# Optimization experiments

Hardware: AMD Instinct MI355X
Metric: run time of the kernel (lower is better)

## Reference

```python
import jax, jax.numpy as jnp
import numpy as np
import math

H = 8  # num_heads
# mock_theta_f Taylor coefficients: K(q) = 1 + q - 2q^2 + 3q^3
COEFFS = (1.0, 1.0, -2.0, 3.0)


def setup_inputs() -> dict:
    key = jax.random.key(0)
    ks = jax.random.split(key, 12)
    B, L, E = 2, 2048, 512
    s = 0.02
    return {
        "query": jax.random.normal(ks[0], (B, L, E), jnp.float32),
        "key_": jax.random.normal(ks[1], (B, L, E), jnp.float32),
        "value": jax.random.normal(ks[2], (B, L, E), jnp.float32),
        "Wq": jax.random.normal(ks[3], (E, E), jnp.float32) * s,
        "bq": jnp.zeros((E,), jnp.float32),
        "Wk": jax.random.normal(ks[4], (E, E), jnp.float32) * s,
        "bk": jnp.zeros((E,), jnp.float32),
        "Wv": jax.random.normal(ks[5], (E, E), jnp.float32) * s,
        "bv": jnp.zeros((E,), jnp.float32),
        "Wo": jax.random.normal(ks[6], (E, E), jnp.float32) * s,
        "bo": jnp.zeros((E,), jnp.float32),
        "log_tau": jnp.zeros((), jnp.float32),  # tau = exp(0) = 1.0
    }


def _horner(q):
    a0, a1, a2, a3 = COEFFS
    val = jnp.full_like(q, a3)
    val = q * val + a2
    val = q * val + a1
    val = q * val + a0
    return jnp.maximum(val, 0.0)


def _attn(query, key_, value, Wq, bq, Wk, bk, Wv, bv, Wo, bo, log_tau):
    B, L, E = query.shape
    S = key_.shape[1]
    Hd = E // H
    scale = math.sqrt(Hd)

    Q = (query @ Wq.T + bq).reshape(B, L, H, Hd).transpose(0, 2, 1, 3)  # (B,H,L,Hd)
    K = (key_ @ Wk.T + bk).reshape(B, S, H, Hd).transpose(0, 2, 1, 3)
    V = (value @ Wv.T + bv).reshape(B, S, H, Hd).transpose(0, 2, 1, 3)

    scores = jnp.einsum("bhld,bhsd->bhls", Q, K) / scale  # (B,H,L,S)

    tau = jnp.exp(log_tau)
    q = jax.nn.sigmoid(scores / tau)
    kv = _horner(q)

    # causal mask (is_causal=True): mask strict upper triangle
    causal = jnp.triu(jnp.ones((L, S), dtype=bool), k=1)  # (L,S)
    kv = jnp.where(causal[None, None], 0.0, kv)

    denom = jnp.sum(kv, axis=-1, keepdims=True)
    weights = kv / jnp.maximum(denom, 1e-12)

    out = jnp.einsum("bhls,bhsd->bhld", weights, V)  # (B,H,L,Hd)
    out = out.transpose(0, 2, 1, 3).reshape(B, L, E)
    return out @ Wo.T + bo


def reference(query, key_, value, Wq, bq, Wk, bk, Wv, bv, Wo, bo, log_tau):
    return _attn(query, key_, value, Wq, bq, Wk, bk, Wv, bv, Wo, bo, log_tau)
```

## Files before the change

### kernel.cpp

```cpp
#include <hip/hip_runtime.h>
#include <hip/hip_bf16.h>


typedef __attribute__((ext_vector_type(8))) __bf16 bf16x8;
typedef __attribute__((ext_vector_type(4))) __bf16 bf16x4;
typedef __attribute__((ext_vector_type(4))) float f32x4;
typedef __attribute__((ext_vector_type(4))) int i32x4;

#define NB 2
#define NL 2048
#define NE 512
#define NH 8
#define HD 64
#define NROW (NB * NL)
#define NJOB 144

__device__ __forceinline__ void gload16(const void* g, void* l) {
  __builtin_amdgcn_global_load_lds(
      (const __attribute__((address_space(1))) void*)g,
      (__attribute__((address_space(3))) void*)l, 16, 0, 0);
}

__global__ __launch_bounds__(256) void cvt_qkv(
    const float* __restrict__ q, const float* __restrict__ k,
    const float* __restrict__ v, __bf16* __restrict__ qo,
    __bf16* __restrict__ ko, __bf16* __restrict__ vo) {
  const int gid = blockIdx.x * 256 + threadIdx.x;
  const int seg = gid >> 19;
  const int i = gid & ((1 << 19) - 1);
  const float* s = seg == 0 ? q : (seg == 1 ? k : v);
  __bf16* d = seg == 0 ? qo : (seg == 1 ? ko : vo);
  float4 x = ((const float4*)s)[i];
  bf16x4 o = {(__bf16)x.x, (__bf16)x.y, (__bf16)x.z, (__bf16)x.w};
  ((bf16x4*)d)[i] = o;
}

__global__ __launch_bounds__(256) void cvt_w(
    const float* __restrict__ w0, const float* __restrict__ w1,
    const float* __restrict__ w2, const float* __restrict__ w3,
    __bf16* __restrict__ o0, __bf16* __restrict__ o1,
    __bf16* __restrict__ o2, __bf16* __restrict__ o3) {
  const int gid = blockIdx.x * 256 + threadIdx.x;
  const int seg = gid >> 16;
  const int i = gid & 0xFFFF;
  const float* s = seg == 0 ? w0 : (seg == 1 ? w1 : (seg == 2 ? w2 : w3));
  __bf16* d = seg == 0 ? o0 : (seg == 1 ? o1 : (seg == 2 ? o2 : o3));
  float4 x = ((const float4*)s)[i];
  bf16x4 o = {(__bf16)x.x, (__bf16)x.y, (__bf16)x.z, (__bf16)x.w};
  ((bf16x4*)d)[i] = o;
}

template <int MODE>
__device__ __forceinline__ void gemm_body(const __bf16* __restrict__ A,
                                          const __bf16* __restrict__ W,
                                          const float* __restrict__ bias,
                                          __bf16* __restrict__ outb,
                                          float* __restrict__ outf) {
  __shared__ __align__(16) __bf16 As[128 * 32];
  __shared__ __align__(16) __bf16 Ws[128 * 32];

  const int tid = threadIdx.x;
  const int lane = tid & 63, w = tid >> 6;
  const int lr = lane & 15, lg = lane >> 4;
  const int brow = blockIdx.y * 128, bcol = blockIdx.x * 128;
  const int wr = (w >> 1) * 64, wc = (w & 1) * 64;

  f32x4 zero4 = {0.f, 0.f, 0.f, 0.f};
  f32x4 acc[4][4];
#pragma unroll
  for (int i = 0; i < 4; ++i)
#pragma unroll
    for (int j = 0; j < 4; ++j) acc[i][j] = zero4;

  const int c0 = tid, c1 = tid + 256;
  const int r0 = c0 >> 2, cc0 = c0 & 3;
  const int r1 = c1 >> 2, cc1 = c1 & 3;

  for (int k0 = 0; k0 < NE; k0 += 32) {
    __syncthreads();
    gload16(A + (size_t)(brow + r0) * NE + k0 + cc0 * 8, As + c0 * 8);
    gload16(W + (size_t)(bcol + r0) * NE + k0 + cc0 * 8, Ws + c0 * 8);
    gload16(A + (size_t)(brow + r1) * NE + k0 + cc1 * 8, As + c1 * 8);
    gload16(W + (size_t)(bcol + r1) * NE + k0 + cc1 * 8, Ws + c1 * 8);
    __syncthreads();

    bf16x8 af[4], wf[4];
#pragma unroll
    for (int mi = 0; mi < 4; ++mi)
      af[mi] = *(const bf16x8*)(As + (wr + mi * 16 + lr) * 32 + lg * 8);
#pragma unroll
    for (int ni = 0; ni < 4; ++ni)
      wf[ni] = *(const bf16x8*)(Ws + (wc + ni * 16 + lr) * 32 + lg * 8);
#pragma unroll
    for (int mi = 0; mi < 4; ++mi)
#pragma unroll
      for (int ni = 0; ni < 4; ++ni)
        acc[mi][ni] = __builtin_amdgcn_mfma_f32_16x16x32_bf16(
            af[mi], wf[ni], acc[mi][ni], 0, 0, 0);
  }

#pragma unroll
  for (int mi = 0; mi < 4; ++mi) {
#pragma unroll
    for (int ni = 0; ni < 4; ++ni) {
      const int col = bcol + wc + ni * 16 + lr;
      const float bv = bias[col];
#pragma unroll
      for (int r = 0; r < 4; ++r) {
        const int row = brow + wr + mi * 16 + lg * 4 + r;
        const float v = acc[mi][ni][r] + bv;
        if (MODE == 0) {
          const int b = row >> 11, l = row & (NL - 1);
          const int h = col >> 6, d = col & 63;
          outb[(((size_t)b * NH + h) * NL + l) * HD + d] = (__bf16)v;
        } else if (MODE == 2) {
          const int b = row >> 11, l = row & (NL - 1);
          const int h = col >> 6, d = col & 63;
          outb[(((size_t)b * NH + h) * HD + d) * NL + l] = (__bf16)v;
        } else {
          outf[(size_t)row * NE + col] = v;
        }
      }
    }
  }
}

__global__ __launch_bounds__(256) void qkv_gemm(
    const __bf16* __restrict__ A0, const __bf16* __restrict__ A1,
    const __bf16* __restrict__ A2, const __bf16* __restrict__ W0,
    const __bf16* __restrict__ W1, const __bf16* __restrict__ W2,
    const float* __restrict__ b0, const float* __restrict__ b1,
    const float* __restrict__ b2, __bf16* __restrict__ O0,
    __bf16* __restrict__ O1, __bf16* __restrict__ O2) {
  const int z = blockIdx.z;
  if (z == 2) {
    gemm_body<2>(A2, W2, b2, O2, nullptr);
  } else {
    const __bf16* A = z == 0 ? A0 : A1;
    const __bf16* W = z == 0 ? W0 : W1;
    const float* bias = z == 0 ? b0 : b1;
    __bf16* O = z == 0 ? O0 : O1;
    gemm_body<0>(A, W, bias, O, nullptr);
  }
}

__global__ __launch_bounds__(256) void out_gemm(const __bf16* __restrict__ A,
                                                const __bf16* __restrict__ W,
                                                const float* __restrict__ bias,
                                                float* __restrict__ outf) {
  gemm_body<1>(A, W, bias, nullptr, outf);
}

template <int SLOTTED>
__global__ __launch_bounds__(256) void attn_kernel(
    const __bf16* __restrict__ Qg, const __bf16* __restrict__ Kg,
    const __bf16* __restrict__ VTg, float* __restrict__ numg,
    float* __restrict__ deng, const float* __restrict__ log_tau) {
  __shared__ __align__(16) __bf16 Kt[64][72];
  __shared__ __align__(16) __bf16 Vt[64][72];

  const int j = blockIdx.x;
  int qb, c;
  if (j < 32) {
    c = 0; qb = j;
  } else if (j < 60) {
    c = 1; qb = j - 28;
  } else if (j < 84) {
    c = 2; qb = j - 52;
  } else if (j < 104) {
    c = 3; qb = j - 72;
  } else if (j < 120) {
    c = 4; qb = j - 88;
  } else if (j < 132) {
    c = 5; qb = j - 100;
  } else if (j < 140) {
    c = 6; qb = j - 108;
  } else {
    c = 7; qb = j - 112;
  }
  const int bh = blockIdx.y;
  const __bf16* Qh = Qg + (size_t)bh * NL * HD;
  const __bf16* Kh = Kg + (size_t)bh * NL * HD;
  const __bf16* Vth = VTg + (size_t)bh * HD * NL;

  const int tid = threadIdx.x;
  const int lane = tid & 63, w = tid >> 6;
  const int lr = lane & 15, lg = lane >> 4;
  const float ninv = -1.44269504f / (8.0f * __expf(log_tau[0]));

  const int q0 = qb * 64;
  const int qg = q0 + w * 16 + lr;
  bf16x8 qf[2];
  qf[0] = *(const bf16x8*)(Qh + (size_t)qg * HD + lg * 8);
  qf[1] = *(const bf16x8*)(Qh + (size_t)qg * HD + 32 + lg * 8);

  f32x4 zero4 = {0.f, 0.f, 0.f, 0.f};
  f32x4 o_acc[4];
#pragma unroll
  for (int n = 0; n < 4; ++n) o_acc[n] = zero4;
  float den_l = 0.f;

  const int t0 = c * 4;
  const int t1 = min(t0 + 4, qb + 1);

  const int kr0 = tid >> 3, kc0 = (tid & 7) * 8;

  bf16x8 kpa = *(const bf16x8*)(Kh + (size_t)(t0 * 64 + kr0) * HD + kc0);
  bf16x8 kpb = *(const bf16x8*)(Kh + (size_t)(t0 * 64 + kr0 + 32) * HD + kc0);
  bf16x8 vpa = *(const bf16x8*)(Vth + (size_t)kr0 * NL + t0 * 64 + kc0);
  bf16x8 vpb = *(const bf16x8*)(Vth + (size_t)(kr0 + 32) * NL + t0 * 64 + kc0);

  const int idxA = (((lane & 16) << 1) + lr) * 4;
  const bool hi = (lane & 32) != 0;

  for (int t = t0; t < t1; ++t) {
    const int kv0 = t * 64;
    __syncthreads();
    *(bf16x8*)&Kt[kr0][kc0] = kpa;
    *(bf16x8*)&Kt[kr0 + 32][kc0] = kpb;
    *(bf16x8*)&Vt[kr0][kc0] = vpa;
    *(bf16x8*)&Vt[kr0 + 32][kc0] = vpb;
    __syncthreads();

    if (t + 1 < t1) {
      const int kn = (t + 1) * 64;
      kpa = *(const bf16x8*)(Kh + (size_t)(kn + kr0) * HD + kc0);
      kpb = *(const bf16x8*)(Kh + (size_t)(kn + kr0 + 32) * HD + kc0);
      vpa = *(const bf16x8*)(Vth + (size_t)kr0 * NL + kn + kc0);
      vpb = *(const bf16x8*)(Vth + (size_t)(kr0 + 32) * NL + kn + kc0);
    }

    f32x4 sacc[4];
#pragma unroll
    for (int si = 0; si < 4; ++si) sacc[si] = zero4;
#pragma unroll
    for (int kk = 0; kk < 2; ++kk) {
#pragma unroll
      for (int si = 0; si < 4; ++si) {
        bf16x8 kf = *(const bf16x8*)&Kt[si * 16 + lr][kk * 32 + lg * 8];
        sacc[si] = __builtin_amdgcn_mfma_f32_16x16x32_bf16(kf, qf[kk],
                                                           sacc[si], 0, 0, 0);
      }
    }

    unsigned pk[4][2];
#pragma unroll
    for (int si = 0; si < 4; ++si) {
      const int sb = kv0 + si * 16 + lg * 4;
      unsigned kbv[4];
#pragma unroll
      for (int r = 0; r < 4; ++r) {
        const float e = __builtin_amdgcn_exp2f(sacc[si][r] * ninv);
        const float qs = __builtin_amdgcn_rcpf(1.0f + e);
        float kvv = fmaf(qs, fmaf(qs, fmaf(qs, 3.0f, -2.0f), 1.0f), 1.0f);
        if (sb + r > qg) kvv = 0.0f;
        const __bf16 kb = (__bf16)kvv;
        den_l += (float)kb;
        kbv[r] = (unsigned)__builtin_bit_cast(unsigned short, kb);
      }
      pk[si][0] = kbv[0] | (kbv[1] << 16);
      pk[si][1] = kbv[2] | (kbv[3] << 16);
    }

#pragma unroll
    for (int kk = 0; kk < 2; ++kk) {
      const int sl = kk * 2, sh = kk * 2 + 1;
      const int a0 = __builtin_amdgcn_ds_bpermute(idxA, (int)pk[sl][0]);
      const int a1 = __builtin_amdgcn_ds_bpermute(idxA, (int)pk[sl][1]);
      const int b0 = __builtin_amdgcn_ds_bpermute(idxA + 64, (int)pk[sl][0]);
      const int b1 = __builtin_amdgcn_ds_bpermute(idxA + 64, (int)pk[sl][1]);
      const int c0 = __builtin_amdgcn_ds_bpermute(idxA, (int)pk[sh][0]);
      const int c1 = __builtin_amdgcn_ds_bpermute(idxA, (int)pk[sh][1]);
      const int d0 = __builtin_amdgcn_ds_bpermute(idxA + 64, (int)pk[sh][0]);
      const int d1 = __builtin_amdgcn_ds_bpermute(idxA + 64, (int)pk[sh][1]);
      i32x4 pw = {hi ? c0 : a0, hi ? c1 : a1, hi ? d0 : b0, hi ? d1 : b1};
      bf16x8 pf = __builtin_bit_cast(bf16x8, pw);
#pragma unroll
      for (int n = 0; n < 4; ++n) {
        bf16x8 vf = *(const bf16x8*)&Vt[n * 16 + lr][kk * 32 + lg * 8];
        o_acc[n] = __builtin_amdgcn_mfma_f32_16x16x32_bf16(pf, vf, o_acc[n],
                                                           0, 0, 0);
      }
    }
  }

  den_l += __shfl_xor(den_l, 16, 64);
  den_l += __shfl_xor(den_l, 32, 64);

  if (SLOTTED) {
    float* nslot = numg + (((size_t)bh * NJOB + j) << 12);
    const int lrow = w * 16 + lg * 4;
    if (lg == 0) {
      float* dslot = deng + (((size_t)bh * NJOB + j) << 6);
      dslot[w * 16 + lr] = den_l;
    }
#pragma unroll
    for (int n = 0; n < 4; ++n) {
      const int col = n * 16 + lr;
#pragma unroll
      for (int r = 0; r < 4; ++r) nslot[(lrow + r) * 64 + col] = o_acc[n][r];
    }
  } else {
    const int orow = q0 + w * 16 + lg * 4;
    if (lg == 0) atomicAdd(&deng[(size_t)bh * NL + q0 + w * 16 + lr], den_l);
#pragma unroll
    for (int n = 0; n < 4; ++n) {
      const int col = n * 16 + lr;
#pragma unroll
      for (int r = 0; r < 4; ++r)
        atomicAdd(&numg[((size_t)bh * NL + orow + r) * HD + col], o_acc[n][r]);
    }
  }
}

__global__ __launch_bounds__(256) void combine_slotted(
    const float* __restrict__ numS, const float* __restrict__ denS,
    __bf16* __restrict__ AO) {
  const int gid = blockIdx.x * 256 + threadIdx.x;
  const int d4 = gid & 15;
  const int row = gid >> 4;
  const int bh = row >> 11, l = row & (NL - 1);
  const int b = bh >> 3, h = bh & 7;
  const int qb = l >> 6, lrow = l & 63;
  const int nc = (qb >> 2) + 1;

  f32x4 acc = {0.f, 0.f, 0.f, 0.f};
  float d = 0.f;
  for (int c = 0; c < nc; ++c) {
    const int jj = qb + 2 * c * (15 - c);
    const size_t sb = (size_t)bh * NJOB + jj;
    acc += *(const f32x4*)(numS + ((sb << 6) + lrow) * 64 + d4 * 4);
    d += denS[(sb << 6) + lrow];
  }
  const float idv = __builtin_amdgcn_rcpf(fmaxf(d, 1e-12f));
  bf16x4 o = {(__bf16)(acc[0] * idv), (__bf16)(acc[1] * idv),
              (__bf16)(acc[2] * idv), (__bf16)(acc[3] * idv)};
  *(bf16x4*)&AO[((size_t)b * NL + l) * NE + h * HD + d4 * 4] = o;
}

__global__ __launch_bounds__(256) void combine_kernel(
    const float* __restrict__ numg, const float* __restrict__ deng,
    __bf16* __restrict__ AO) {
  const int gid = blockIdx.x * 256 + threadIdx.x;
  const int d4 = gid & 15;
  const int row = gid >> 4;
  const int bh = row >> 11, l = row & (NL - 1);
  const int b = bh >> 3, h = bh & 7;
  f32x4 n4 = ((const f32x4*)numg)[gid];
  const float idv = __builtin_amdgcn_rcpf(fmaxf(deng[row], 1e-12f));
  bf16x4 o = {(__bf16)(n4[0] * idv), (__bf16)(n4[1] * idv),
              (__bf16)(n4[2] * idv), (__bf16)(n4[3] * idv)};
  *(bf16x4*)&AO[((size_t)b * NL + l) * NE + h * HD + d4 * 4] = o;
}

extern "C" void kernel_launch(void* const* d_in, const int* in_sizes, int n_in,
                              void* d_out, int out_size, void* d_ws,
                              size_t ws_size, hipStream_t stream) {
  const float* query = (const float*)d_in[0];
  const float* key_ = (const float*)d_in[1];
  const float* value = (const float*)d_in[2];
  const float* Wq = (const float*)d_in[3];
  const float* bq = (const float*)d_in[4];
  const float* Wk = (const float*)d_in[5];
  const float* bk = (const float*)d_in[6];
  const float* Wv = (const float*)d_in[7];
  const float* bv = (const float*)d_in[8];
  const float* Wo = (const float*)d_in[9];
  const float* bo = (const float*)d_in[10];
  const float* log_tau = (const float*)d_in[11];

  char* ws = (char*)d_ws;
  const size_t MB = 1024 * 1024;
  const bool slotted = (ws_size >= 55 * MB);

  __bf16* xb = (__bf16*)(ws + 0 * MB);
  __bf16* kxb = (__bf16*)(ws + 4 * MB);
  __bf16* vxb = (__bf16*)(ws + 8 * MB);

  __bf16 *wqb, *wkb, *wvb, *wob, *Qh, *Kh, *VT, *AO;
  float *numb, *denb;
  if (slotted) {
    numb = (float*)(ws + 0 * MB);
    denb = (float*)(ws + 36 * MB);
    wqb = (__bf16*)(ws + 37 * MB);
    wkb = (__bf16*)(ws + 37 * MB + 512 * 1024);
    wvb = (__bf16*)(ws + 38 * MB);
    wob = (__bf16*)(ws + 38 * MB + 512 * 1024);
    Qh = (__bf16*)(ws + 39 * MB);
    Kh = (__bf16*)(ws + 43 * MB);
    VT = (__bf16*)(ws + 47 * MB);
    AO = (__bf16*)(ws + 51 * MB);
  } else {
    numb = (float*)(ws + 0 * MB);
    denb = (float*)(ws + 8 * MB);
    wqb = (__bf16*)(ws + 12 * MB);
    wkb = (__bf16*)(ws + 12 * MB + 512 * 1024);
    wvb = (__bf16*)(ws + 13 * MB);
    wob = (__bf16*)(ws + 13 * MB + 512 * 1024);
    Qh = (__bf16*)(ws + 14 * MB);
    Kh = (__bf16*)(ws + 18 * MB);
    VT = (__bf16*)(ws + 22 * MB);
    AO = (__bf16*)(ws + 26 * MB);
  }

  cvt_qkv<<<3 * (1 << 19) / 256, 256, 0, stream>>>(query, key_, value, xb, kxb,
                                                   vxb);
  cvt_w<<<4 * (1 << 16) / 256, 256, 0, stream>>>(Wq, Wk, Wv, Wo, wqb, wkb, wvb,
                                                 wob);

  dim3 gq(NE / 128, NROW / 128, 3);
  qkv_gemm<<<gq, 256, 0, stream>>>(xb, kxb, vxb, wqb, wkb, wvb, bq, bk, bv, Qh,
                                   Kh, VT);

  dim3 ga(NJOB, NB * NH);
  if (slotted) {
    attn_kernel<1><<<ga, 256, 0, stream>>>(Qh, Kh, VT, numb, denb, log_tau);
    combine_slotted<<<2048, 256, 0, stream>>>(numb, denb, AO);
  } else {
    hipMemsetAsync(ws, 0, 8 * MB + 128 * 1024, stream);
    attn_kernel<0><<<ga, 256, 0, stream>>>(Qh, Kh, VT, numb, denb, log_tau);
    combine_kernel<<<2048, 256, 0, stream>>>(numb, denb, AO);
  }

  dim3 gg(NE / 128, NROW / 128);
  out_gemm<<<gg, 256, 0, stream>>>(AO, wob, bo, (float*)d_out);
}
```

Measured before the change: 79.57 us.

## Process two query blocks per attention workgroup to reuse staged K/V tiles

New measurement: 83.53 us. 5.0% more time.

```diff
diff --git a/kernel.cpp b/kernel.cpp
--- a/kernel.cpp
+++ b/kernel.cpp
@@ -159,25 +159,18 @@
   __shared__ __align__(16) __bf16 Kt[64][72];
   __shared__ __align__(16) __bf16 Vt[64][72];
 
-  const int j = blockIdx.x;
-  int qb, c;
-  if (j < 32) {
-    c = 0; qb = j;
-  } else if (j < 60) {
-    c = 1; qb = j - 28;
-  } else if (j < 84) {
-    c = 2; qb = j - 52;
-  } else if (j < 104) {
-    c = 3; qb = j - 72;
-  } else if (j < 120) {
-    c = 4; qb = j - 88;
-  } else if (j < 132) {
-    c = 5; qb = j - 100;
-  } else if (j < 140) {
-    c = 6; qb = j - 108;
-  } else {
-    c = 7; qb = j - 112;
-  }
+  int jj = 71 - blockIdx.x;
+  int qi = 0, c = 0;
+  for (int k = 0; k < 16; ++k) {
+    const int n = (k >> 1) + 1;
+    if (jj < n) { qi = k; c = jj; break; }
+    jj -= n;
+  }
+  const int m2 = qi >> 1;
+  const int job = ((qi & 1) ? (m2 + 1) * (m2 + 1) : m2 * (m2 + 1)) + c;
+  const int qA = 2 * qi;
+  const int q0B = (qA + 1) * 64;
+
   const int bh = blockIdx.y;
   const __bf16* Qh = Qg + (size_t)bh * NL * HD;
   const __bf16* Kh = Kg + (size_t)bh * NL * HD;
@@ -188,20 +181,24 @@
   const int lr = lane & 15, lg = lane >> 4;
   const float ninv = -1.44269504f / (8.0f * __expf(log_tau[0]));
 
-  const int q0 = qb * 64;
-  const int qg = q0 + w * 16 + lr;
-  bf16x8 qf[2];
-  qf[0] = *(const bf16x8*)(Qh + (size_t)qg * HD + lg * 8);
-  qf[1] = *(const bf16x8*)(Qh + (size_t)qg * HD + 32 + lg * 8);
+  bf16x8 qf[2][2];
+#pragma unroll
+  for (int pp = 0; pp < 2; ++pp) {
+    const int qrow = q0B - pp * 64 + w * 16 + lr;
+    qf[pp][0] = *(const bf16x8*)(Qh + (size_t)qrow * HD + lg * 8);
+    qf[pp][1] = *(const bf16x8*)(Qh + (size_t)qrow * HD + 32 + lg * 8);
+  }
 
   f32x4 zero4 = {0.f, 0.f, 0.f, 0.f};
-  f32x4 o_acc[4];
-#pragma unroll
-  for (int n = 0; n < 4; ++n) o_acc[n] = zero4;
-  float den_l = 0.f;
+  f32x4 o_acc[2][4];
+#pragma unroll
+  for (int pp = 0; pp < 2; ++pp)
+#pragma unroll
+    for (int n = 0; n < 4; ++n) o_acc[pp][n] = zero4;
+  float den_l[2] = {0.f, 0.f};
 
   const int t0 = c * 4;
-  const int t1 = min(t0 + 4, qb + 1);
+  const int t1 = min(t0 + 4, 2 * qi + 2);
 
   const int kr0 = tid >> 3, kc0 = (tid & 7) * 8;
 
@@ -230,85 +227,105 @@
       vpb = *(const bf16x8*)(Vth + (size_t)(kr0 + 32) * NL + kn + kc0);
     }
 
-    f32x4 sacc[4];
-#pragma unroll
-    for (int si = 0; si < 4; ++si) sacc[si] = zero4;
-#pragma unroll
-    for (int kk = 0; kk < 2; ++kk) {
+#pragma unroll
+    for (int pp = 0; pp < 2; ++pp) {
+      if (pp == 1 && t > qA) continue;
+      const int qq = q0B - pp * 64 + w * 16 + lr;
+
+      f32x4 sacc[4];
+#pragma unroll
+      for (int si = 0; si < 4; ++si) sacc[si] = zero4;
+#pragma unroll
+      for (int kk = 0; kk < 2; ++kk) {
+#pragma unroll
+        for (int si = 0; si < 4; ++si) {
+          bf16x8 kf = *(const bf16x8*)&Kt[si * 16 + lr][kk * 32 + lg * 8];
+          sacc[si] = __builtin_amdgcn_mfma_f32_16x16x32_bf16(
+              kf, qf[pp][kk], sacc[si], 0, 0, 0);
+        }
+      }
+
+      unsigned pk[4][2];
 #pragma unroll
       for (int si = 0; si < 4; ++si) {
-        bf16x8 kf = *(const bf16x8*)&Kt[si * 16 + lr][kk * 32 + lg * 8];
-        sacc[si] = __builtin_amdgcn_mfma_f32_16x16x32_bf16(kf, qf[kk],
-                                                           sacc[si], 0, 0, 0);
+        const int sb = kv0 + si * 16 + lg * 4;
+        unsigned kbv[4];
+#pragma unroll
+        for (int r = 0; r < 4; ++r) {
+          const float e = __builtin_amdgcn_exp2f(sacc[si][r] * ninv);
+          const float qs = __builtin_amdgcn_rcpf(1.0f + e);
+          float kvv = fmaf(qs, fmaf(qs, fmaf(qs, 3.0f, -2.0f), 1.0f), 1.0f);
+          if (sb + r > qq) kvv = 0.0f;
+          const __bf16 kb = (__bf16)kvv;
+          den_l[pp] += (float)kb;
+          kbv[r] = (unsigned)__builtin_bit_cast(unsigned short, kb);
+        }
+        pk[si][0] = kbv[0] | (kbv[1] << 16);
+        pk[si][1] = kbv[2] | (kbv[3] << 16);
+      }
+
+#pragma unroll
+      for (int kk = 0; kk < 2; ++kk) {
+        const int sl = kk * 2, sh = kk * 2 + 1;
+        const int a0 = __builtin_amdgcn_ds_bpermute(idxA, (int)pk[sl][0]);
+        const int a1 = __builtin_amdgcn_ds_bpermute(idxA, (int)pk[sl][1]);
+        const int b0 = __builtin_amdgcn_ds_bpermute(idxA + 64, (int)pk[sl][0]);
+        const int b1 = __builtin_amdgcn_ds_bpermute(idxA + 64, (int)pk[sl][1]);
+        const int c0 = __builtin_amdgcn_ds_bpermute(idxA, (int)pk[sh][0]);
+        const int c1 = __builtin_amdgcn_ds_bpermute(idxA, (int)pk[sh][1]);
+        const int d0 = __builtin_amdgcn_ds_bpermute(idxA + 64, (int)pk[sh][0]);
+        const int d1 = __builtin_amdgcn_ds_bpermute(idxA + 64, (int)pk[sh][1]);
+        i32x4 pw = {hi ? c0 : a0, hi ? c1 : a1, hi ? d0 : b0, hi ? d1 : b1};
+        bf16x8 pf = __builtin_bit_cast(bf16x8, pw);
+#pragma unroll
+        for (int n = 0; n < 4; ++n) {
+          bf16x8 vf = *(const bf16x8*)&Vt[n * 16 + lr][kk * 32 + lg * 8];
+          o_acc[pp][n] = __builtin_amdgcn_mfma_f32_16x16x32_bf16(
+              pf, vf, o_acc[pp][n], 0, 0, 0);
+        }
       }
     }
-
-    unsigned pk[4][2];
-#pragma unroll
-    for (int si = 0; si < 4; ++si) {
-      const int sb = kv0 + si * 16 + lg * 4;
-      unsigned kbv[4];
-#pragma unroll
-      for (int r = 0; r < 4; ++r) {
-        const float e = __builtin_amdgcn_exp2f(sacc[si][r] * ninv);
-        const float qs = __builtin_amdgcn_rcpf(1.0f + e);
-        float kvv = fmaf(qs, fmaf(qs, fmaf(qs, 3.0f, -2.0f), 1.0f), 1.0f);
-        if (sb + r > qg) kvv = 0.0f;
-        const __bf16 kb = (__bf16)kvv;
-        den_l += (float)kb;
-        kbv[r] = (unsigned)__builtin_bit_cast(unsigned short, kb);
-      }
-      pk[si][0] = kbv[0] | (kbv[1] << 16);
-      pk[si][1] = kbv[2] | (kbv[3] << 16);
-    }
-
-#pragma unroll
-    for (int kk = 0; kk < 2; ++kk) {
-      const int sl = kk * 2, sh = kk * 2 + 1;
-      const int a0 = __builtin_amdgcn_ds_bpermute(idxA, (int)pk[sl][0]);
-      const int a1 = __builtin_amdgcn_ds_bpermute(idxA, (int)pk[sl][1]);
-      const int b0 = __builtin_amdgcn_ds_bpermute(idxA + 64, (int)pk[sl][0]);
-      const int b1 = __builtin_amdgcn_ds_bpermute(idxA + 64, (int)pk[sl][1]);
-      const int c0 = __builtin_amdgcn_ds_bpermute(idxA, (int)pk[sh][0]);
-      const int c1 = __builtin_amdgcn_ds_bpermute(idxA, (int)pk[sh][1]);
-      const int d0 = __builtin_amdgcn_ds_bpermute(idxA + 64, (int)pk[sh][0]);
-      const int d1 = __builtin_amdgcn_ds_bpermute(idxA + 64, (int)pk[sh][1]);
-      i32x4 pw = {hi ? c0 : a0, hi ? c1 : a1, hi ? d0 : b0, hi ? d1 : b1};
-      bf16x8 pf = __builtin_bit_cast(bf16x8, pw);
+  }
+
+#pragma unroll
+  for (int pp = 0; pp < 2; ++pp) {
+    den_l[pp] += __shfl_xor(den_l[pp], 16, 64);
+    den_l[pp] += __shfl_xor(den_l[pp], 32, 64);
+  }
+
+  if (SLOTTED) {
+#pragma unroll
+    for (int pp = 0; pp < 2; ++pp) {
+      const int slot = 2 * job + 1 - pp;
+      float* nslot = numg + (((size_t)bh * NJOB + slot) << 12);
+      const int lrow = w * 16 + lg * 4;
+      if (lg == 0) {
+        float* dslot = deng + (((size_t)bh * NJOB + slot) << 6);
+        dslot[w * 16 + lr] = den_l[pp];
+      }
 #pragma unroll
       for (int n = 0; n < 4; ++n) {
-        bf16x8 vf = *(const bf16x8*)&Vt[n * 16 + lr][kk * 32 + lg * 8];
-        o_acc[n] = __builtin_amdgcn_mfma_f32_16x16x32_bf16(pf, vf, o_acc[n],
-                                                           0, 0, 0);
-      }
-    }
-  }
-
-  den_l += __shfl_xor(den_l, 16, 64);
-  den_l += __shfl_xor(den_l, 32, 64);
-
-  if (SLOTTED) {
-    float* nslot = numg + (((size_t)bh * NJOB + j) << 12);
-    const int lrow = w * 16 + lg * 4;
-    if (lg == 0) {
-      float* dslot = deng + (((size_t)bh * NJOB + j) << 6);
-      dslot[w * 16 + lr] = den_l;
-    }
-#pragma unroll
-    for (int n = 0; n < 4; ++n) {
-      const int col = n * 16 + lr;
-#pragma unroll
-      for (int r = 0; r < 4; ++r) nslot[(lrow + r) * 64 + col] = o_acc[n][r];
+        const int col = n * 16 + lr;
+#pragma unroll
+        for (int r = 0; r < 4; ++r)
+          nslot[(lrow + r) * 64 + col] = o_acc[pp][n][r];
+      }
     }
   } else {
-    const int orow = q0 + w * 16 + lg * 4;
-    if (lg == 0) atomicAdd(&deng[(size_t)bh * NL + q0 + w * 16 + lr], den_l);
-#pragma unroll
-    for (int n = 0; n < 4; ++n) {
-      const int col = n * 16 + lr;
-#pragma unroll
-      for (int r = 0; r < 4; ++r)
-        atomicAdd(&numg[((size_t)bh * NL + orow + r) * HD + col], o_acc[n][r]);
+#pragma unroll
+    for (int pp = 0; pp < 2; ++pp) {
+      const int orow = q0B - pp * 64 + w * 16 + lg * 4;
+      if (lg == 0)
+        atomicAdd(&deng[(size_t)bh * NL + q0B - pp * 64 + w * 16 + lr],
+                  den_l[pp]);
+#pragma unroll
+      for (int n = 0; n < 4; ++n) {
+        const int col = n * 16 + lr;
+#pragma unroll
+        for (int r = 0; r < 4; ++r)
+          atomicAdd(&numg[((size_t)bh * NL + orow + r) * HD + col],
+                    o_acc[pp][n][r]);
+      }
     }
   }
 }
@@ -322,13 +339,15 @@
   const int bh = row >> 11, l = row & (NL - 1);
   const int b = bh >> 3, h = bh & 7;
   const int qb = l >> 6, lrow = l & 63;
+  const int qi = qb >> 1, par = qb & 1, m2 = qi >> 1;
+  const int jbase = (qi & 1) ? (m2 + 1) * (m2 + 1) : m2 * (m2 + 1);
   const int nc = (qb >> 2) + 1;
 
   f32x4 acc = {0.f, 0.f, 0.f, 0.f};
   float d = 0.f;
   for (int c = 0; c < nc; ++c) {
-    const int jj = qb + 2 * c * (15 - c);
-    const size_t sb = (size_t)bh * NJOB + jj;
+    const int slot = 2 * (jbase + c) + par;
+    const size_t sb = (size_t)bh * NJOB + slot;
     acc += *(const f32x4*)(numS + ((sb << 6) + lrow) * 64 + d4 * 4);
     d += denS[(sb << 6) + lrow];
   }
@@ -412,7 +431,7 @@
   qkv_gemm<<<gq, 256, 0, stream>>>(xb, kxb, vxb, wqb, wkb, wvb, bq, bk, bv, Qh,
                                    Kh, VT);
 
-  dim3 ga(NJOB, NB * NH);
+  dim3 ga(72, NB * NH);
   if (slotted) {
     attn_kernel<1><<<ga, 256, 0, stream>>>(Qh, Kh, VT, numb, denb, log_tau);
     combine_slotted<<<2048, 256, 0, stream>>>(numb, denb, AO);
```
